# Performance work log

Hardware: AMD Instinct MI355X
Metric: run time of the kernel (lower is better)

The kernel has to match this reference:

```python
import jax, jax.numpy as jnp
from jax import lax
import numpy as np

EPS = 1e-5
K = 16
NUM_GROUP = 128
D = 384
HEADS = 6
DEPTH = 4
BETA = 0.25

def gelu(x):
    return jax.nn.gelu(x, approximate=False)

def linear(x, w, b):
    return x @ w.T + b

def layer_norm(x, g, b):
    mu = x.mean(-1, keepdims=True)
    var = x.var(-1, keepdims=True)
    return (x - mu) / jnp.sqrt(var + EPS) * g + b

def group_norm(x, gamma, beta, groups):
    B, C = x.shape[0], x.shape[1]
    sp = x.shape[2:]
    xg = x.reshape((B, groups, C // groups) + sp)
    axes = tuple(range(2, xg.ndim))
    mu = xg.mean(axes, keepdims=True)
    var = xg.var(axes, keepdims=True)
    xg = (xg - mu) / jnp.sqrt(var + EPS)
    x = xg.reshape((B, C) + sp)
    shp = (1, C) + (1,) * len(sp)
    return x * gamma.reshape(shp) + beta.reshape(shp)

def knn_idx(q, kp, k):
    # q [B,Nq,3], kp [B,Nk,3] -> idx [B,Nq,k] of k nearest keys
    d = jnp.sum(q * q, -1)[:, :, None] - 2.0 * jnp.einsum('bqd,bkd->bqk', q, kp) + jnp.sum(kp * kp, -1)[:, None, :]
    _, idx = lax.top_k(-d, k)
    return idx

def graph_feature(coor_q, x_q, coor_k, x_k, k):
    # coor [B,3,N], x [B,C,N] -> [B,2C,Nq,k]
    idx = knn_idx(coor_q.transpose(0, 2, 1), coor_k.transpose(0, 2, 1), k)
    feat = jax.vmap(lambda a, i: a[:, i])(x_k, idx)  # [B,C,Nq,k]
    xq = x_q[:, :, :, None]
    return jnp.concatenate([feat - xq, jnp.broadcast_to(xq, feat.shape)], axis=1)

def fps_indices(xyz, m):
    # farthest point sampling, start at index 0 (matches pointnet2)
    B, N, _ = xyz.shape
    def body(carry, _):
        dist, far = carry
        c = jnp.take_along_axis(xyz, far[:, None, None], axis=1)
        d = jnp.sum((xyz - c) ** 2, -1)
        dist = jnp.minimum(dist, d)
        return (dist, jnp.argmax(dist, -1).astype(jnp.int32)), far
    init = (jnp.full((B, N), 1e10, xyz.dtype), jnp.zeros((B,), jnp.int32))
    _, idxs = lax.scan(body, init, None, length=m)
    return idxs.T  # [B,m]

def gather_ch(x, idx):
    return jax.vmap(lambda a, i: a[:, i])(x, idx)

def conv1x1_2d(x, w):
    return jnp.einsum('oc,bcnk->bonk', w, x)

def conv1x1_1d(x, w, b):
    return jnp.einsum('oc,bcn->bon', w, x) + b[None, :, None]

def linear_resize(x, out_len):
    # F.interpolate(mode='linear', align_corners=False) along axis 1 of [B,N,D]
    n = x.shape[1]
    pos = (jnp.arange(out_len, dtype=x.dtype) + 0.5) * (n / out_len) - 0.5
    pos = jnp.clip(pos, 0.0, n - 1.0)
    i0 = jnp.floor(pos).astype(jnp.int32)
    i1 = jnp.minimum(i0 + 1, n - 1)
    w = (pos - i0.astype(x.dtype))[None, :, None]
    return x[:, i0] * (1.0 - w) + x[:, i1] * w

def vq(z, cb, beta):
    d = jnp.sum(z * z, -1, keepdims=True) - 2.0 * (z @ cb.T) + jnp.sum(cb * cb, -1)
    eidx = jnp.argmin(d, -1)
    q = cb[eidx]
    loss = jnp.mean((lax.stop_gradient(z) - q) ** 2) + beta * jnp.mean((z - lax.stop_gradient(q)) ** 2)
    q_st = z + lax.stop_gradient(q - z)  # straight-through
    return q_st, loss, eidx

def forward_core(xyz, it_w, it_b, g1_w, g1_g, g1_bt, g2_w, g2_g, g2_bt, g3_w, g3_g, g3_bt, g4_w, g4_g, g4_bt, pe_w1, pe_b1, pe_w2, pe_b2, ip_w1, ip_b1, ip_w2, ip_b2, ln1_g, ln1_b, qkv_w, qkv_b, o_w, o_b, ln2_g, ln2_b, m1_w, m1_b, m2_w, m2_b, pyr_w1, pyr_b1, pyr_g1, pyr_bt1, pyr_w2, pyr_b2, pyr_g2, pyr_bt2, fus_w, fus_b, cb0, cb1, cb2):
    B = xyz.shape[0]
    x = xyz.transpose(0, 2, 1)  # [B,7,N]
    coor, normal, plane = x[:, :3], x[:, 3:6], x[:, 6:7]
    f = conv1x1_1d(coor, it_w, it_b)  # [B,8,N]

    def edge_conv(cq, fq, ck, fk, w, g, bt, groups):
        h = graph_feature(cq, fq, ck, fk, K)
        h = conv1x1_2d(h, w)
        h = group_norm(h, g, bt, groups)
        h = jnp.where(h > 0, h, 0.2 * h)  # LeakyReLU(0.2)
        return h.max(axis=-1)

    f = edge_conv(coor, f, coor, f, g1_w, g1_g, g1_bt, 4)  # [B,32,N]
    idx = fps_indices(coor.transpose(0, 2, 1), NUM_GROUP)
    coor_q, normal_q, plane_q, f_q = gather_ch(coor, idx), gather_ch(normal, idx), gather_ch(plane, idx), gather_ch(f, idx)
    f = edge_conv(coor_q, f_q, coor, f, g2_w, g2_g, g2_bt, 4)  # [B,64,128]
    coor, normal, plane = coor_q, normal_q, plane_q
    f = edge_conv(coor, f, coor, f, g3_w, g3_g, g3_bt, 4)  # [B,64,128]
    idx = fps_indices(coor.transpose(0, 2, 1), NUM_GROUP)
    coor_q, normal_q, plane_q, f_q = gather_ch(coor, idx), gather_ch(normal, idx), gather_ch(plane, idx), gather_ch(f, idx)
    f = edge_conv(coor_q, f_q, coor, f, g4_w, g4_g, g4_bt, 4)  # [B,128,128]
    coor = coor_q.transpose(0, 2, 1)  # [B,128,3]
    f = f.transpose(0, 2, 1)          # [B,128,128]

    pe = linear(gelu(linear(coor, pe_w1, pe_b1)), pe_w2, pe_b2)
    h = linear(gelu(linear(f, ip_w1, ip_b1)), ip_w2, ip_b2)
    t = h + pe
    hd = D // HEADS
    scale = 1.0 / np.sqrt(hd)
    N = t.shape[1]
    for l in range(DEPTH):
        hn = layer_norm(t, ln1_g[l], ln1_b[l])
        qkv = hn @ qkv_w[l] + qkv_b[l]
        q, k_, v = jnp.split(qkv, 3, axis=-1)
        q = q.reshape(B, N, HEADS, hd)
        k_ = k_.reshape(B, N, HEADS, hd)
        v = v.reshape(B, N, HEADS, hd)
        att = jax.nn.softmax(jnp.einsum('bqhd,bkhd->bhqk', q, k_) * scale, axis=-1)
        o = jnp.einsum('bhqk,bkhd->bqhd', att, v).reshape(B, N, D)
        t = t + o @ o_w[l] + o_b[l]
        hn = layer_norm(t, ln2_g[l], ln2_b[l])
        t = t + gelu(hn @ m1_w[l] + m1_b[l]) @ m2_w[l] + m2_b[l]

    base = t  # [B,128,384]
    cbs = (cb0, cb1, cb2)
    outs, losses, idxs = [], [], []
    prev = None
    for level in range(3):
        res = max(base.shape[1] // (2 ** level), 8)
        if res == base.shape[1]:
            lf = base
        else:
            # adaptive_avg_pool1d with evenly dividing bins == reshape-mean
            lf = base.reshape(B, res, base.shape[1] // res, D).mean(2)
        c = lf.transpose(0, 2, 1)
        c = gelu(group_norm(conv1x1_1d(c, pyr_w1[level], pyr_b1[level]), pyr_g1[level], pyr_bt1[level], 8))
        c = gelu(group_norm(conv1x1_1d(c, pyr_w2[level], pyr_b2[level]), pyr_g2[level], pyr_bt2[level], 8))
        proc = c.transpose(0, 2, 1)
        if level > 0:
            pu = prev if prev.shape[1] == res else linear_resize(prev, res)
            proc = gelu(linear(jnp.concatenate([proc, pu], axis=-1), fus_w[level - 1], fus_b[level - 1]))
        q_st, loss, eidx = vq(proc, cbs[level], BETA)
        outs.append(q_st)
        losses.append(loss)
        idxs.append(eidx)
        prev = q_st
    return outs, losses, idxs

def setup_inputs():
    key = jax.random.key(0)
    cnt = [0]
    def nrm(shape, s=0.02):
        cnt[0] += 1
        return jax.random.normal(jax.random.fold_in(key, cnt[0]), shape, jnp.float32) * s
    L = 4
    inp = {}
    inp['xyz'] = nrm((8, 4096, 7), 1.0)
    inp['it_w'] = nrm((8, 3), 0.3)
    inp['it_b'] = jnp.zeros((8,), jnp.float32)
    inp['g1_w'] = nrm((32, 16), 0.1); inp['g1_g'] = jnp.ones((32,)); inp['g1_bt'] = jnp.zeros((32,))
    inp['g2_w'] = nrm((64, 64), 0.1); inp['g2_g'] = jnp.ones((64,)); inp['g2_bt'] = jnp.zeros((64,))
    inp['g3_w'] = nrm((64, 128), 0.1); inp['g3_g'] = jnp.ones((64,)); inp['g3_bt'] = jnp.zeros((64,))
    inp['g4_w'] = nrm((128, 128), 0.1); inp['g4_g'] = jnp.ones((128,)); inp['g4_bt'] = jnp.zeros((128,))
    inp['pe_w1'] = nrm((128, 3), 0.3); inp['pe_b1'] = jnp.zeros((128,))
    inp['pe_w2'] = nrm((D, 128), 0.05); inp['pe_b2'] = jnp.zeros((D,))
    inp['ip_w1'] = nrm((512, 128), 0.05); inp['ip_b1'] = jnp.zeros((512,))
    inp['ip_w2'] = nrm((D, 512), 0.03); inp['ip_b2'] = jnp.zeros((D,))
    inp['ln1_g'] = jnp.ones((L, D)); inp['ln1_b'] = jnp.zeros((L, D))
    inp['qkv_w'] = nrm((L, D, 3 * D)); inp['qkv_b'] = jnp.zeros((L, 3 * D))
    inp['o_w'] = nrm((L, D, D)); inp['o_b'] = jnp.zeros((L, D))
    inp['ln2_g'] = jnp.ones((L, D)); inp['ln2_b'] = jnp.zeros((L, D))
    inp['m1_w'] = nrm((L, D, 4 * D)); inp['m1_b'] = jnp.zeros((L, 4 * D))
    inp['m2_w'] = nrm((L, 4 * D, D)); inp['m2_b'] = jnp.zeros((L, D))
    inp['pyr_w1'] = nrm((3, 2 * D, D), 0.03); inp['pyr_b1'] = jnp.zeros((3, 2 * D))
    inp['pyr_g1'] = jnp.ones((3, 2 * D)); inp['pyr_bt1'] = jnp.zeros((3, 2 * D))
    inp['pyr_w2'] = nrm((3, D, 2 * D), 0.03); inp['pyr_b2'] = jnp.zeros((3, D))
    inp['pyr_g2'] = jnp.ones((3, D)); inp['pyr_bt2'] = jnp.zeros((3, D))
    inp['fus_w'] = nrm((2, D, 2 * D), 0.03); inp['fus_b'] = jnp.zeros((2, D))
    inp['cb0'] = nrm((8192, D), 0.5)
    inp['cb1'] = nrm((4096, D), 0.5)
    inp['cb2'] = nrm((2048, D), 0.5)
    return inp

def reference(xyz, it_w, it_b, g1_w, g1_g, g1_bt, g2_w, g2_g, g2_bt, g3_w, g3_g, g3_bt, g4_w, g4_g, g4_bt, pe_w1, pe_b1, pe_w2, pe_b2, ip_w1, ip_b1, ip_w2, ip_b2, ln1_g, ln1_b, qkv_w, qkv_b, o_w, o_b, ln2_g, ln2_b, m1_w, m1_b, m2_w, m2_b, pyr_w1, pyr_b1, pyr_g1, pyr_bt1, pyr_w2, pyr_b2, pyr_g2, pyr_bt2, fus_w, fus_b, cb0, cb1, cb2):
    outs, losses, idxs = forward_core(xyz, it_w, it_b, g1_w, g1_g, g1_bt, g2_w, g2_g, g2_bt, g3_w, g3_g, g3_bt, g4_w, g4_g, g4_bt, pe_w1, pe_b1, pe_w2, pe_b2, ip_w1, ip_b1, ip_w2, ip_b2, ln1_g, ln1_b, qkv_w, qkv_b, o_w, o_b, ln2_g, ln2_b, m1_w, m1_b, m2_w, m2_b, pyr_w1, pyr_b1, pyr_g1, pyr_bt1, pyr_w2, pyr_b2, pyr_g2, pyr_bt2, fus_w, fus_b, cb0, cb1, cb2)
    # concat quantized features of the 3 levels (128+64+32 tokens), total VQ loss, per-level indices
    return (jnp.concatenate(outs, axis=1), losses[0] + losses[1] + losses[2], idxs[0], idxs[1], idxs[2])
```

## Files before the change

### kernel.cpp

```cpp
#include <hip/hip_runtime.h>
#include <math.h>

#define EPSF 1e-5f

__device__ __forceinline__ float geluf(float x){
  return 0.5f*x*(1.0f + erff(x*0.70710678118654752440f));
}

typedef __attribute__((ext_vector_type(8))) short bf16x8;
typedef __attribute__((ext_vector_type(4))) float f32x4;

constexpr size_t WQKV = 0;
constexpr size_t WO   = WQKV + (size_t)4*1152*384;
constexpr size_t WM1  = WO   + (size_t)4*384*384;
constexpr size_t WM2  = WM1  + (size_t)4*1536*384;
constexpr size_t WIP1 = WM2  + (size_t)4*384*1536;
constexpr size_t WIP2 = WIP1 + (size_t)512*128;
constexpr size_t WPE2 = WIP2 + (size_t)384*512;
constexpr size_t WPY1 = WPE2 + (size_t)384*128;
constexpr size_t WPY2 = WPY1 + (size_t)3*768*384;
constexpr size_t WFUS = WPY2 + (size_t)3*384*768;
constexpr size_t WTOT = WFUS + (size_t)2*384*768;

__device__ __forceinline__ void split_rne(float x, short& h, short& l){
// ... 195 lines not shown
    if(d0 <= tau0){
      int slot = atomicAdd(&scnt[wave][0], 1);
      if(slot < 64){ scd[wave][0][slot] = d0; sci[wave][0][slot] = n; }
    }
    if(d1 <= tau1){
      int slot = atomicAdd(&scnt[wave][1], 1);
      if(slot < 64){ scd[wave][1][slot] = d1; sci[wave][1][slot] = n; }
    }
  }
  __syncthreads();

  #pragma unroll
  for(int qq=0; qq<2; qq++){
    int cnt = scnt[wave][qq];
    int* orow = idxout + ((size_t)b*Nq + nq0 + qq)*KNN_K;
    float nqx = qq ? q1x : q0x;
    float nqy = qq ? q1y : q0y;
    float nqz = qq ? q1z : q0z;
    if(cnt <= 64){
      float d = (lane < cnt) ? scd[wave][qq][lane] : INFINITY;
      int  id = (lane < cnt) ? sci[wave][qq][lane] : 0x7fffffff;
      #pragma unroll
      for(int k=2;k<=64;k<<=1){
        #pragma unroll
        for(int j=k>>1;j>=1;j>>=1){
          float od = __shfl_xor(d, j, 64);
          int oi = __shfl_xor(id, j, 64);
          bool lower = (lane & j)==0;
          bool asc = (lane & k)==0;
          bool otherSmaller = (od < d) || (od==d && oi < id);
          if((lower==asc) == otherSmaller){ d = od; id = oi; }
        }
      }
      if(lane < KNN_K) orow[lane] = id;
    } else {
      float bd[KNN_K]; int bi2[KNN_K];
      #pragma unroll
      for(int j=0;j<KNN_K;j++){ bd[j]=INFINITY; bi2[j]=0x7fffffff; }
      float curmax = INFINITY;
      for(int n=lane; n<Nk; n+=64){
        float4 k4 = sk[n];
        float d = fmaf(nqx, k4.x, fmaf(nqy, k4.y, fmaf(nqz, k4.z, k4.w)));
        if(d < curmax){
          int pm = 0; float md = bd[0]; int mi = bi2[0];
          #pragma unroll
          for(int j=1;j<KNN_K;j++){
            if(bd[j] > md || (bd[j]==md && bi2[j] > mi)){ md=bd[j]; mi=bi2[j]; pm=j; }
          }
          #pragma unroll
          for(int j=0;j<KNN_K;j++){ if(j==pm){ bd[j]=d; bi2[j]=n; } }
          float m2 = -INFINITY;
          #pragma unroll
          for(int j=0;j<KNN_K;j++) m2 = fmaxf(m2, bd[j]);
          curmax = m2;
        }
      }
      for(int t=0;t<KNN_K;t++){
        float ld = bd[0]; int li_ = bi2[0];
        #pragma unroll
        for(int j=1;j<KNN_K;j++){
          if(bd[j] < ld || (bd[j]==ld && bi2[j] < li_)){ ld=bd[j]; li_=bi2[j]; }
        }
        float wd = ld; int wi = li_;
        #pragma unroll
        for(int m=1;m<64;m<<=1){
          float od = __shfl_xor(wd, m, 64);
          int oi = __shfl_xor(wi, m, 64);
          if(od < wd || (od==wd && oi < wi)){ wd=od; wi=oi; }
        }
        if(ld==wd && li_==wi){
          #pragma unroll
          for(int j=0;j<KNN_K;j++){ if(bd[j]==wd && bi2[j]==wi){ bd[j]=INFINITY; bi2[j]=0x7fffffff; } }
        }
        if(lane==0) orow[t] = wi;
      }
    }
  }
}

template<int NMAX, int PPT, int NT>
__global__ __launch_bounds__(NT) void fps_kernel(const float* __restrict__ coor, int* __restrict__ out,
                                                 int N, int M){
  __shared__ float skx[NMAX], sky[NMAX], skz[NMAX];
  __shared__ unsigned long long swk[NT/64];
  constexpr int NW = NT/64;
  int b = blockIdx.x;
  int tid = threadIdx.x;
  int lane = tid & 63, wid = tid >> 6;
  const float* cx = coor + (size_t)b*3*N;
  const float* cy = cx + N;
  const float* cz = cx + 2*N;
  float px[PPT], py[PPT], pz[PPT], dist[PPT];
  #pragma unroll
  for(int j=0;j<PPT;j++){
    int n = tid + j*NT;
    float x = cx[n], y = cy[n], z = cz[n];
    px[j]=x; py[j]=y; pz[j]=z; dist[j]=1e10f;
    skx[n]=x; sky[n]=y; skz[n]=z;
  }
  if(tid==0) out[b*M] = 0;
  __syncthreads();
  float fx = skx[0], fy = sky[0], fz = skz[0];
  for(int t=1;t<M;t++){
    unsigned long long bk = 0ull;
    #pragma unroll
    for(int j=0;j<PPT;j++){
      int n = tid + j*NT;
      float dx = __fsub_rn(px[j], fx);
      float dy = __fsub_rn(py[j], fy);
      float dz = __fsub_rn(pz[j], fz);
      float d = __fadd_rn(__fadd_rn(__fmul_rn(dx,dx), __fmul_rn(dy,dy)), __fmul_rn(dz,dz));
      float nd = fminf(dist[j], d);
      dist[j] = nd;
      union{float f; unsigned u;} db; db.f = nd;
      unsigned long long key = ((unsigned long long)db.u << 32) | (unsigned)(0x7fffffff - n);
      bk = (key > bk) ? key : bk;
    }
    #pragma unroll
    for(int m=1;m<64;m<<=1){
      unsigned long long ok = __shfl_xor(bk, m, 64);
      bk = (ok > bk) ? ok : bk;
    }
    if(lane==0) swk[wid] = bk;
    __syncthreads();
    unsigned long long g = swk[0];
    #pragma unroll
    for(int w=1;w<NW;w++){ unsigned long long o = swk[w]; g = (o > g) ? o : g; }
    int wi = 0x7fffffff - (int)(unsigned)(g & 0xffffffffull);
    if(tid==0) out[b*M + t] = wi;
    fx = skx[wi]; fy = sky[wi]; fz = skz[wi];
    __syncthreads();
  }
}

template<int CIN, int COUT>
__global__ __launch_bounds__(256) void ec_main(const float* __restrict__ fQ, const float* __restrict__ fK,
    const int* __restrict__ idx, const float* __restrict__ W,
    float* __restrict__ hmax_out, float* __restrict__ part, int Nq, int Nk)
{
  constexpr int CG = COUT/4;
  __shared__ float sW1t[CIN][COUT];
  __shared__ float sWdt[CIN][COUT];
  __shared__ float ps[4], pq[4];
  if(threadIdx.x < 4){ ps[threadIdx.x]=0.f; pq[threadIdx.x]=0.f; }
  for(int i=threadIdx.x;i<CIN*COUT;i+=256){
    int c = i % COUT, p = i / COUT;
    float w1 = W[c*2*CIN + p];
    sW1t[p][c] = w1;
    sWdt[p][c] = W[c*2*CIN + CIN + p] - w1;
  }
  __syncthreads();
  int gid = blockIdx.x*256 + threadIdx.x;
  int c = gid % COUT;
  int t = gid / COUT;
  int n = t % Nq;
  int b = t / Nq;
  const float* fq = fQ + ((size_t)b*Nq + n)*CIN;
  float t2 = 0.f;
  #pragma unroll
  for(int p=0;p<CIN;p++) t2 = fmaf(sWdt[p][c], fq[p], t2);
  const int* idr = idx + ((size_t)b*Nq+n)*16;
  const float* fkb = fK + (size_t)b*Nk*CIN;
  float hmax = -INFINITY, s = 0.f, q = 0.f;
  for(int k=0;k<16;k++){
    int nb = idr[k];
    const float* fk = fkb + (size_t)nb*CIN;
    float h = t2;
    #pragma unroll
    for(int p=0;p<CIN;p++) h = fmaf(sW1t[p][c], fk[p], h);
    hmax = fmaxf(hmax, h);
    s += h;
    q = fmaf(h,h,q);
  }
  hmax_out[((size_t)b*Nq + n)*COUT + c] = hmax;
  #pragma unroll
  for(int m=1;m<CG;m<<=1){ s += __shfl_xor(s,m,64); q += __shfl_xor(q,m,64); }
  if((threadIdx.x & (CG-1)) == 0){
    int grp = c / CG;
    atomicAdd(&ps[grp], s);
    atomicAdd(&pq[grp], q);
  }
  __syncthreads();
  if(threadIdx.x < 4){
    part[(size_t)blockIdx.x*8 + threadIdx.x*2+0] = ps[threadIdx.x];
    part[(size_t)blockIdx.x*8 + threadIdx.x*2+1] = pq[threadIdx.x];
  }
}

__global__ __launch_bounds__(256) void ec_reduce(const float* __restrict__ part, float* __restrict__ mr,
                                                 int nblk_per_b, float invcnt){
  int b = blockIdx.x >> 2, g = blockIdx.x & 3;
  const float* p = part + (size_t)b*nblk_per_b*8 + g*2;
  float s=0.f, q=0.f;
  for(int i=threadIdx.x;i<nblk_per_b;i+=256){ s += p[(size_t)i*8]; q += p[(size_t)i*8+1]; }
  __shared__ float rs[256], rq[256];
  rs[threadIdx.x]=s; rq[threadIdx.x]=q; __syncthreads();
  for(int st=128;st>0;st>>=1){
    if(threadIdx.x<st){ rs[threadIdx.x]+=rs[threadIdx.x+st]; rq[threadIdx.x]+=rq[threadIdx.x+st]; }
    __syncthreads();
  }
  if(threadIdx.x==0){
    float mean = rs[0]*invcnt;
    float var = rq[0]*invcnt - mean*mean; var = fmaxf(var, 0.f);
    mr[blockIdx.x*2+0] = mean;
    mr[blockIdx.x*2+1] = 1.0f/sqrtf(var + EPSF);
  }
}

__global__ void ec_norm(float* __restrict__ h, const float* __restrict__ mr, const float* __restrict__ gamma,
                        const float* __restrict__ beta, int Nq, int COUT, int total){
  int i = blockIdx.x*blockDim.x + threadIdx.x;
  if(i >= total) return;
  int c = i % COUT;
  int b = i/(Nq*COUT);
// ... 3 lines not shown
  h[i] = v > 0.f ? v : 0.2f*v;
}

__global__ __launch_bounds__(128) void gemm64(const float* __restrict__ A, const float* __restrict__ Bm,
    const float* __restrict__ bias, float* __restrict__ C,
    int M, int N, int K, int BT, int act, int addto)
{
  __shared__ float As[16][64];
  __shared__ float Bs[16][64];
  int t = threadIdx.x;
  int tx = t & 15, ty = t >> 4;
  int bm = blockIdx.y*64, bn = blockIdx.x*64;
  float acc[8][4] = {{0.f}};
  int kvec = ((K & 15) == 0);
  for(int k0 = 0; k0 < K; k0 += 16){
    #pragma unroll
    for(int i=0;i<2;i++){
      int id = t*2 + i;
      int row = id >> 2, q = id & 3;
      if(kvec){
        float4 av = *(const float4*)(A + (size_t)(bm+row)*K + k0 + q*4);
        As[q*4+0][row]=av.x; As[q*4+1][row]=av.y; As[q*4+2][row]=av.z; As[q*4+3][row]=av.w;
      } else {
        #pragma unroll
        for(int j=0;j<4;j++){
          int kk = k0 + q*4 + j;
          As[q*4+j][row] = (kk < K) ? A[(size_t)(bm+row)*K + kk] : 0.f;
        }
      }
    }
    #pragma unroll
    for(int i=0;i<2;i++){
      int id = t*2 + i;
      if(BT){
        int col = id >> 2, q = id & 3;
        if(kvec){
          float4 bv = *(const float4*)(Bm + (size_t)(bn+col)*K + k0 + q*4);
          Bs[q*4+0][col]=bv.x; Bs[q*4+1][col]=bv.y; Bs[q*4+2][col]=bv.z; Bs[q*4+3][col]=bv.w;
        } else {
          #pragma unroll
          for(int j=0;j<4;j++){
            int kk = k0 + q*4 + j;
            Bs[q*4+j][col] = (kk < K) ? Bm[(size_t)(bn+col)*K + kk] : 0.f;
          }
        }
      } else {
        int kr = id >> 4, cq = (id & 15)*4;
        if(k0+kr < K){
          *(float4*)&Bs[kr][cq] = *(const float4*)(Bm + (size_t)(k0+kr)*N + bn + cq);
        } else {
          Bs[kr][cq]=0.f; Bs[kr][cq+1]=0.f; Bs[kr][cq+2]=0.f; Bs[kr][cq+3]=0.f;
        }
      }
    }
    __syncthreads();
    #pragma unroll
    for(int kk=0;kk<16;kk++){
      float4 a0 = *(const float4*)&As[kk][ty*8];
      float4 a1 = *(const float4*)&As[kk][ty*8+4];
      float4 b  = *(const float4*)&Bs[kk][tx*4];
      float av[8]; float bv[4];
      *(float4*)&av[0] = a0; *(float4*)&av[4] = a1; *(float4*)&bv[0] = b;
      #pragma unroll
      for(int r=0;r<8;r++){
        #pragma unroll
        for(int c2=0;c2<4;c2++) acc[r][c2] = fmaf(av[r], bv[c2], acc[r][c2]);
      }
    }
    __syncthreads();
  }
  float4 bb = make_float4(0.f,0.f,0.f,0.f);
  if(bias) bb = *(const float4*)(bias + bn + tx*4);
  #pragma unroll
  for(int r=0;r<8;r++){
    int row = bm + ty*8 + r;
    float4 v = make_float4(acc[r][0]+bb.x, acc[r][1]+bb.y, acc[r][2]+bb.z, acc[r][3]+bb.w);
    if(act==1){ v.x=geluf(v.x); v.y=geluf(v.y); v.z=geluf(v.z); v.w=geluf(v.w); }
    float* Cp = C + (size_t)row*N + bn + tx*4;
    if(addto){ float4 o = *(const float4*)Cp; v.x+=o.x; v.y+=o.y; v.z+=o.z; v.w+=o.w; }
    *(float4*)Cp = v;
  }
}

__global__ __launch_bounds__(256) void ln_stats(const float* __restrict__ x, float* __restrict__ mr, int D){
  int row = blockIdx.x*4 + (threadIdx.x >> 6);
  int lane = threadIdx.x & 63;
  const float* xr = x + (size_t)row*D;
  float s = 0.f;
  for(int i=lane;i<D;i+=64) s += xr[i];
  #pragma unroll
  for(int m=1;m<64;m<<=1) s += __shfl_xor(s, m, 64);
  float mu = s/(float)D;
  float q = 0.f;
  for(int i=lane;i<D;i+=64){ float d = xr[i]-mu; q += d*d; }
  #pragma unroll
  for(int m=1;m<64;m<<=1) q += __shfl_xor(q, m, 64);
  if(lane==0){
    mr[row*2+0] = mu;
    mr[row*2+1] = 1.0f/sqrtf(q/(float)D + EPSF);
  }
}

__global__ __launch_bounds__(256) void gemm_mfma(const float* __restrict__ A, const float* __restrict__ Bm,
    const float* __restrict__ bias, float* __restrict__ C,
    int M, int N, int K, int BT, int act, int addto,
    const float* __restrict__ lnmr, const float* __restrict__ lng, const float* __restrict__ lnb)
{
  __shared__ short sAhi[64][72];
  __shared__ short sAlo[64][72];
  __shared__ short sBhi[64][72];
  __shared__ short sBlo[64][72];
  int t = threadIdx.x;
  int lane = t & 63, wave = t >> 6;
  int wm = wave >> 1, wn = wave & 1;
  int g = lane >> 4, rr = lane & 15;
  int bm = blockIdx.y*64, bn = blockIdx.x*64;
  f32x4 acc[2][2];
  #pragma unroll
  for(int m=0;m<2;m++)
    #pragma unroll
    for(int n=0;n<2;n++)
      #pragma unroll
      for(int r=0;r<4;r++) acc[m][n][r] = 0.f;

  int ar_ = t >> 2, akq = (t & 3)*16;
  int bc_ = BT ? (t >> 2) : (t & 63);
  int bkq = BT ? ((t & 3)*16) : ((t >> 6)*16);
  float lmu = 0.f, lrstd = 0.f;
  if(lnmr){ lmu = lnmr[(bm+ar_)*2+0]; lrstd = lnmr[(bm+ar_)*2+1]; }

  float areg[16], breg[16];
  auto loadA = [&](int k0){
    const float* ap = A + (size_t)(bm + ar_)*K + k0 + akq;
    *(float4*)&areg[0]  = *(const float4*)(ap);
    *(float4*)&areg[4]  = *(const float4*)(ap+4);
    *(float4*)&areg[8]  = *(const float4*)(ap+8);
    *(float4*)&areg[12] = *(const float4*)(ap+12);
  };
  auto loadB = [&](int k0){
    if(BT){
      const float* bp = Bm + (size_t)(bn + bc_)*K + k0 + bkq;
      *(float4*)&breg[0]  = *(const float4*)(bp);
      *(float4*)&breg[4]  = *(const float4*)(bp+4);
      *(float4*)&breg[8]  = *(const float4*)(bp+8);
      *(float4*)&breg[12] = *(const float4*)(bp+12);
    } else {
      #pragma unroll
      for(int j=0;j<16;j++) breg[j] = Bm[(size_t)(k0 + bkq + j)*N + bn + bc_];
    }
  };
  auto stageA = [&](int k0){
    #pragma unroll
    for(int v8=0; v8<2; v8++){
      bf16x8 h, l;
      #pragma unroll
      for(int j=0;j<8;j++){
        float x = areg[v8*8+j];
        if(lnmr){
          int kk = k0 + akq + v8*8 + j;
          x = (x - lmu)*lrstd*lng[kk] + lnb[kk];
        }
        short th, tl;
        split_rne(x, th, tl);
        h[j] = th; l[j] = tl;
      }
      *(bf16x8*)&sAhi[ar_][akq + v8*8] = h;
      *(bf16x8*)&sAlo[ar_][akq + v8*8] = l;
    }
  };
  auto stageB = [&](){
    #pragma unroll
    for(int v8=0; v8<2; v8++){
      bf16x8 h, l;
      #pragma unroll
      for(int j=0;j<8;j++){
        short th, tl;
        split_rne(breg[v8*8+j], th, tl);
        h[j] = th; l[j] = tl;
      }
      *(bf16x8*)&sBhi[bc_][bkq + v8*8] = h;
      *(bf16x8*)&sBlo[bc_][bkq + v8*8] = l;
    }
  };

  loadA(0); loadB(0);
  int nk = K >> 6;
  for(int ki=0; ki<nk; ki++){
    stageA(ki*64); stageB();
    __syncthreads();
    if(ki+1 < nk){ loadA((ki+1)*64); loadB((ki+1)*64); }
    #pragma unroll
    for(int half=0; half<2; half++){
      bf16x8 ah[2], al[2], bh[2], bl[2];
      #pragma unroll
      for(int m=0;m<2;m++){
        int arow = wm*32 + m*16 + rr;
        ah[m] = *(bf16x8*)&sAhi[arow][half*32 + g*8];
        al[m] = *(bf16x8*)&sAlo[arow][half*32 + g*8];
      }
      #pragma unroll
      for(int n=0;n<2;n++){
        int bcol = wn*32 + n*16 + rr;
        bh[n] = *(bf16x8*)&sBhi[bcol][half*32 + g*8];
        bl[n] = *(bf16x8*)&sBlo[bcol][half*32 + g*8];
      }
      #pragma unroll
      for(int m=0;m<2;m++){
        #pragma unroll
        for(int n=0;n<2;n++){
          acc[m][n] = __builtin_amdgcn_mfma_f32_16x16x32_bf16(ah[m], bh[n], acc[m][n], 0, 0, 0);
          acc[m][n] = __builtin_amdgcn_mfma_f32_16x16x32_bf16(ah[m], bl[n], acc[m][n], 0, 0, 0);
          acc[m][n] = __builtin_amdgcn_mfma_f32_16x16x32_bf16(al[m], bh[n], acc[m][n], 0, 0, 0);
        }
      }
    }
    __syncthreads();
  }
  #pragma unroll
  for(int n=0;n<2;n++){
    int col = bn + wn*32 + n*16 + rr;
    float bb = bias ? bias[col] : 0.f;
    #pragma unroll
    for(int m=0;m<2;m++){
      #pragma unroll
      for(int r4=0;r4<4;r4++){
        int row = bm + wm*32 + m*16 + g*4 + r4;
        float v = acc[m][n][r4] + bb;
        if(act==1) v = geluf(v);
        size_t o = (size_t)row*N + col;
        if(addto) v += C[o];
        C[o] = v;
      }
    }
  }
}

__global__ __launch_bounds__(256) void gemm_mfma_ps(const float* __restrict__ A,
    const short* __restrict__ Bhi, const short* __restrict__ Blo,
    const float* __restrict__ bias, float* __restrict__ C,
    int M, int N, int K, int act, int addto,
    const float* __restrict__ lnmr, const float* __restrict__ lng, const float* __restrict__ lnb)
{
  __shared__ short sAhi[64][72];
  __shared__ short sAlo[64][72];
  __shared__ short sBhi[64][72];
  __shared__ short sBlo[64][72];
  int t = threadIdx.x;
  int lane = t & 63, wave = t >> 6;
  int wm = wave >> 1, wn = wave & 1;
  int g = lane >> 4, rr = lane & 15;
  int bm = blockIdx.y*64, bn = blockIdx.x*64;
  f32x4 acc[2][2];
  #pragma unroll
  for(int m=0;m<2;m++)
    #pragma unroll
    for(int n=0;n<2;n++)
      #pragma unroll
      for(int r=0;r<4;r++) acc[m][n][r] = 0.f;

  int ar_ = t >> 2, akq = (t & 3)*16;
  float lmu = 0.f, lrstd = 0.f;
  if(lnmr){ lmu = lnmr[(bm+ar_)*2+0]; lrstd = lnmr[(bm+ar_)*2+1]; }

  float areg[16];
  bf16x8 pbh[2], pbl[2];
  auto loadA = [&](int k0){
    const float* ap = A + (size_t)(bm + ar_)*K + k0 + akq;
    *(float4*)&areg[0]  = *(const float4*)(ap);
    *(float4*)&areg[4]  = *(const float4*)(ap+4);
    *(float4*)&areg[8]  = *(const float4*)(ap+8);
    *(float4*)&areg[12] = *(const float4*)(ap+12);
  };
  auto loadB = [&](int k0){
    const short* hp = Bhi + (size_t)(bn + ar_)*K + k0 + akq;
    const short* lp = Blo + (size_t)(bn + ar_)*K + k0 + akq;
    pbh[0] = *(const bf16x8*)hp; pbh[1] = *(const bf16x8*)(hp+8);
    pbl[0] = *(const bf16x8*)lp; pbl[1] = *(const bf16x8*)(lp+8);
  };
  auto stageA = [&](int k0){
    #pragma unroll
    for(int v8=0; v8<2; v8++){
      bf16x8 h, l;
      #pragma unroll
      for(int j=0;j<8;j++){
        float x = areg[v8*8+j];
        if(lnmr){
          int kk = k0 + akq + v8*8 + j;
          x = (x - lmu)*lrstd*lng[kk] + lnb[kk];
        }
        short th, tl;
        split_rne(x, th, tl);
        h[j] = th; l[j] = tl;
      }
      *(bf16x8*)&sAhi[ar_][akq + v8*8] = h;
      *(bf16x8*)&sAlo[ar_][akq + v8*8] = l;
    }
  };
  auto stageB = [&](){
    *(bf16x8*)&sBhi[ar_][akq]   = pbh[0];
    *(bf16x8*)&sBhi[ar_][akq+8] = pbh[1];
    *(bf16x8*)&sBlo[ar_][akq]   = pbl[0];
    *(bf16x8*)&sBlo[ar_][akq+8] = pbl[1];
  };

  loadA(0); loadB(0);
  int nk = K >> 6;
  for(int ki=0; ki<nk; ki++){
    stageA(ki*64); stageB();
    __syncthreads();
    if(ki+1 < nk){ loadA((ki+1)*64); loadB((ki+1)*64); }
    #pragma unroll
    for(int half=0; half<2; half++){
      bf16x8 ah[2], al[2], bh[2], bl[2];
      #pragma unroll
      for(int m=0;m<2;m++){
        int arow = wm*32 + m*16 + rr;
        ah[m] = *(bf16x8*)&sAhi[arow][half*32 + g*8];
        al[m] = *(bf16x8*)&sAlo[arow][half*32 + g*8];
      }
      #pragma unroll
      for(int n=0;n<2;n++){
        int bcol = wn*32 + n*16 + rr;
        bh[n] = *(bf16x8*)&sBhi[bcol][half*32 + g*8];
        bl[n] = *(bf16x8*)&sBlo[bcol][half*32 + g*8];
      }
      #pragma unroll
      for(int m=0;m<2;m++){
        #pragma unroll
        for(int n=0;n<2;n++){
          acc[m][n] = __builtin_amdgcn_mfma_f32_16x16x32_bf16(ah[m], bh[n], acc[m][n], 0, 0, 0);
          acc[m][n] = __builtin_amdgcn_mfma_f32_16x16x32_bf16(ah[m], bl[n], acc[m][n], 0, 0, 0);
          acc[m][n] = __builtin_amdgcn_mfma_f32_16x16x32_bf16(al[m], bh[n], acc[m][n], 0, 0, 0);
        }
      }
    }
    __syncthreads();
  }
  #pragma unroll
  for(int n=0;n<2;n++){
    int col = bn + wn*32 + n*16 + rr;
    float bb = bias ? bias[col] : 0.f;
    #pragma unroll
    for(int m=0;m<2;m++){
      #pragma unroll
      for(int r4=0;r4<4;r4++){
        int row = bm + wm*32 + m*16 + g*4 + r4;
        float v = acc[m][n][r4] + bb;
        if(act==1) v = geluf(v);
        size_t o = (size_t)row*N + col;
        if(addto) v += C[o];
        C[o] = v;
      }
    }
  }
}

__global__ __launch_bounds__(256) void gemm_vq(const short* __restrict__ Ahi, const short* __restrict__ Alo,
    const short* __restrict__ Bhi, const short* __restrict__ Blo,
    const float* __restrict__ cbsq, unsigned long long* __restrict__ keys, int M, int N, int K)
{
  __shared__ short sAhi[64][72];
  __shared__ short sAlo[64][72];
  __shared__ short sBhi[64][72];
  __shared__ short sBlo[64][72];
  int t = threadIdx.x;
  int lane = t & 63, wave = t >> 6;
  int wm = wave >> 1, wn = wave & 1;
  int g = lane >> 4, rr = lane & 15;
  int bm = blockIdx.y*64, bn = blockIdx.x*64;
// ... 263 lines not shown
  const float* pyr_w2 = (const float*)d_in[39];
  const float* pyr_b2 = (const float*)d_in[40];
  const float* pyr_g2 = (const float*)d_in[41];
  const float* pyr_bt2= (const float*)d_in[42];
  const float* fus_w  = (const float*)d_in[43];
  const float* fus_b  = (const float*)d_in[44];
  const float* cb0    = (const float*)d_in[45];
  const float* cb1    = (const float*)d_in[46];
  const float* cb2    = (const float*)d_in[47];

  float* ws  = (float*)d_ws;
  float* out = (float*)d_out;

  constexpr int B_ = 8, N0 = 4096, M0 = 128;
  constexpr size_t OFF_COOR0 = 0;
  constexpr size_t OFF_F0    = OFF_COOR0 + (size_t)B_*3*N0;
  constexpr size_t OFF_F1    = OFF_F0 + (size_t)B_*8*N0;
  constexpr size_t OFF_IDX1  = OFF_F1 + (size_t)B_*32*N0;
  constexpr size_t OFF_FPS1  = OFF_IDX1 + (size_t)B_*N0*16;
  constexpr size_t OFF_COOR1 = OFF_FPS1 + B_*M0;
  constexpr size_t OFF_F1Q   = OFF_COOR1 + B_*3*M0;
  constexpr size_t OFF_IDX2  = OFF_F1Q + B_*32*M0;
  constexpr size_t OFF_F2    = OFF_IDX2 + (size_t)B_*M0*16;
  constexpr size_t OFF_IDX3  = OFF_F2 + B_*64*M0;
  constexpr size_t OFF_F3    = OFF_IDX3 + (size_t)B_*M0*16;
  constexpr size_t OFF_FPS2  = OFF_F3 + B_*64*M0;
  constexpr size_t OFF_COOR2 = OFF_FPS2 + B_*M0;
  constexpr size_t OFF_F3Q   = OFF_COOR2 + B_*3*M0;
  constexpr size_t OFF_IDX4  = OFF_F3Q + B_*64*M0;
  constexpr size_t OFF_F4    = OFF_IDX4 + (size_t)B_*M0*16;
  constexpr size_t OFF_COORT = OFF_F4 + B_*128*M0;
  constexpr size_t OFF_TMP   = OFF_COORT + B_*M0*3;
  constexpr size_t OFF_T     = OFF_TMP + (size_t)1024*512;
  constexpr size_t OFF_QKV   = OFF_T + (size_t)1024*384;
  constexpr size_t OFF_ATT   = OFF_QKV + (size_t)1024*1152;
  constexpr size_t OFF_MID   = OFF_ATT + (size_t)1024*384;
  constexpr size_t OFF_LF    = OFF_MID + (size_t)1024*1536;
  constexpr size_t OFF_C1    = OFF_LF + (size_t)512*384;
  constexpr size_t OFF_C2    = OFF_C1 + (size_t)1024*768;
  constexpr size_t OFF_CAT   = OFF_C2 + (size_t)1024*384;
  constexpr size_t OFF_PROC  = OFF_CAT + (size_t)512*768;
  constexpr size_t OFF_KEYS  = OFF_PROC + (size_t)512*384;
  constexpr size_t OFF_LNMR  = OFF_KEYS + 3584;
  constexpr size_t OFF_CBSQ  = OFF_LNMR + 2048;
  constexpr size_t OFF_PART  = OFF_CBSQ + 14336;
  constexpr size_t OFF_MR    = OFF_PART + 32768;
  constexpr size_t OFF_LOSS  = OFF_MR + 64;
  constexpr size_t OFF_ZHI   = OFF_LOSS + 64;
  constexpr size_t OFF_ZLO   = OFF_ZHI + 196608;
  constexpr size_t OFF_CBHI  = OFF_ZLO + 196608;
  constexpr size_t OFF_CBLO  = OFF_CBHI + 2752512;
  constexpr size_t OFF_WHI = OFF_CBLO + 2752512;
  constexpr size_t OFF_WLO = OFF_WHI + (WTOT+1)/2;
  constexpr size_t OFF_END = OFF_WLO + (WTOT+1)/2;

  float* coor0 = ws + OFF_COOR0;
  float* f0    = ws + OFF_F0;
  float* f1    = ws + OFF_F1;
  int*   idx1  = (int*)(ws + OFF_IDX1);
  int*   fps1  = (int*)(ws + OFF_FPS1);
  float* coor1 = ws + OFF_COOR1;
  float* f1q   = ws + OFF_F1Q;
  int*   idx2  = (int*)(ws + OFF_IDX2);
  float* f2    = ws + OFF_F2;
  int*   idx3  = (int*)(ws + OFF_IDX3);
  float* f3    = ws + OFF_F3;
  int*   fps2  = (int*)(ws + OFF_FPS2);
  float* coor2 = ws + OFF_COOR2;
  float* f3q   = ws + OFF_F3Q;
  int*   idx4  = (int*)(ws + OFF_IDX4);
  float* f4    = ws + OFF_F4;
  float* coorT = ws + OFF_COORT;
  float* tmp   = ws + OFF_TMP;
  float* tbuf  = ws + OFF_T;
  float* qkvb  = ws + OFF_QKV;
  float* attb  = ws + OFF_ATT;
  float* midb  = ws + OFF_MID;
  float* lfb   = ws + OFF_LF;
  float* c1b   = ws + OFF_C1;
  float* c2b   = ws + OFF_C2;
  float* catb  = ws + OFF_CAT;
  float* procb = ws + OFF_PROC;
  unsigned long long* keys = (unsigned long long*)(ws + OFF_KEYS);
  float* lnst  = ws + OFF_LNMR;
  float* cbsq  = ws + OFF_CBSQ;
  float* part  = ws + OFF_PART;
  float* mr    = ws + OFF_MR;
  float* lossa = ws + OFF_LOSS;
  short* zhi   = (short*)(ws + OFF_ZHI);
  short* zlo   = (short*)(ws + OFF_ZLO);
  short* cbhi  = (short*)(ws + OFF_CBHI);
  short* cblo  = (short*)(ws + OFF_CBLO);
  short* whi   = (short*)(ws + OFF_WHI);
  short* wlo   = (short*)(ws + OFF_WLO);

  bool presplit = ws_size >= OFF_END * sizeof(float);

  auto cdiv = [](int a, int b){ return (a+b-1)/b; };
  auto gemm_full = [&](const float* A, const float* Bm, const float* bias, float* C,
                       int M, int N, int K, int BT, int act, int addto,
                       const float* lnmr, const float* lng, const float* lnb){
    if(((K & 63) == 0) && ((N & 63) == 0) && ((M & 63) == 0)){
      dim3 g(N/64, M/64);
      gemm_mfma<<<g, 256, 0, stream>>>(A, Bm, bias, C, M, N, K, BT, act, addto, lnmr, lng, lnb);
    } else {
      dim3 g(N/64, M/64), blk(128);
      gemm64<<<g, blk, 0, stream>>>(A, Bm, bias, C, M, N, K, BT, act, addto);
    }
  };
  auto gemmW = [&](const float* A, const float* W, size_t wofs, const float* bias, float* C,
                   int M, int N, int K, int BT, int act, int addto,
                   const float* lnmr, const float* lng, const float* lnb){
    if(presplit && ((K & 63) == 0) && ((N & 63) == 0) && ((M & 63) == 0)){
      dim3 g(N/64, M/64);
      gemm_mfma_ps<<<g, 256, 0, stream>>>(A, whi + wofs, wlo + wofs, bias, C, M, N, K, act, addto, lnmr, lng, lnb);
    } else {
      gemm_full(A, W, bias, C, M, N, K, BT, act, addto, lnmr, lng, lnb);
    }
  };

  hipMemsetAsync(lossa, 0, 8*sizeof(float), stream);
  hipMemsetAsync(keys, 0xFF, 1792*sizeof(unsigned long long), stream);

  init_pts<<<cdiv(B_*N0,256),256,0,stream>>>(xyz, it_w, it_b, coor0, f0, B_, N0);

  split_cb3<<<cdiv(14336*384/4,256),256,0,stream>>>(cb0, cb1, cb2, cbhi, cblo);
  cbsq3<<<cdiv(14336,256),256,0,stream>>>(cb0, cb1, cb2, cbsq);

  if(presplit){
    transpose_split<<<dim3(1152/32,384/32,4),256,0,stream>>>(qkv_w, whi+WQKV, wlo+WQKV, 384, 1152,
        (size_t)384*1152, (size_t)1152*384);
    transpose_split<<<dim3(384/32,384/32,4),256,0,stream>>>(o_w, whi+WO, wlo+WO, 384, 384,
        (size_t)384*384, (size_t)384*384);
    transpose_split<<<dim3(1536/32,384/32,4),256,0,stream>>>(m1_w, whi+WM1, wlo+WM1, 384, 1536,
        (size_t)384*1536, (size_t)1536*384);
    transpose_split<<<dim3(384/32,1536/32,4),256,0,stream>>>(m2_w, whi+WM2, wlo+WM2, 1536, 384,
        (size_t)1536*384, (size_t)384*1536);
    int totq = (512*128 + 384*512 + 384*128 + 3*768*384 + 3*384*768 + 2*384*768)/4;
    split_multi<<<cdiv(totq,256),256,0,stream>>>(ip_w1, ip_w2, pe_w2, pyr_w1, pyr_w2, fus_w, whi, wlo);
  }

  knn2q_kernel<4096,512><<<B_*N0/16,512,0,stream>>>(coor0, coor0, idx1, B_, N0, N0);
  ec_main<8,32><<<B_*32*N0/256,256,0,stream>>>(f0, f0, idx1, g1_w, f1, part, N0, N0);
  ec_reduce<<<32,256,0,stream>>>(part, mr, 32*N0/256, 1.0f/(8.0f*N0*16.0f));
  ec_norm<<<cdiv(B_*32*N0,256),256,0,stream>>>(f1, mr, g1_g, g1_bt, N0, 32, B_*32*N0);

  fps_kernel<4096,8,512><<<B_,512,0,stream>>>(coor0, fps1, N0, M0);
  gather_ch_kernel<<<cdiv(B_*3*M0,256),256,0,stream>>>(coor0, fps1, coor1, B_, 3, N0, M0);
  gather_rows<<<cdiv(B_*M0*32,256),256,0,stream>>>(f1, fps1, f1q, B_, 32, N0, M0);

  knn2q_kernel<4096,512><<<B_*M0/16,512,0,stream>>>(coor1, coor0, idx2, B_, M0, N0);
  ec_main<32,64><<<B_*64*M0/256,256,0,stream>>>(f1q, f1, idx2, g2_w, f2, part, M0, N0);
  ec_reduce<<<32,256,0,stream>>>(part, mr, 64*M0/256, 1.0f/(16.0f*M0*16.0f));
  ec_norm<<<cdiv(B_*64*M0,256),256,0,stream>>>(f2, mr, g2_g, g2_bt, M0, 64, B_*64*M0);

  knn2q_kernel<128,512><<<B_*M0/16,512,0,stream>>>(coor1, coor1, idx3, B_, M0, M0);
  ec_main<64,64><<<B_*64*M0/256,256,0,stream>>>(f2, f2, idx3, g3_w, f3, part, M0, M0);
  ec_reduce<<<32,256,0,stream>>>(part, mr, 64*M0/256, 1.0f/(16.0f*M0*16.0f));
  ec_norm<<<cdiv(B_*64*M0,256),256,0,stream>>>(f3, mr, g3_g, g3_bt, M0, 64, B_*64*M0);

  fps_kernel<128,1,128><<<B_,128,0,stream>>>(coor1, fps2, M0, M0);
  gather_ch_kernel<<<cdiv(B_*3*M0,256),256,0,stream>>>(coor1, fps2, coor2, B_, 3, M0, M0);
  gather_rows<<<cdiv(B_*M0*64,256),256,0,stream>>>(f3, fps2, f3q, B_, 64, M0, M0);

  knn2q_kernel<128,512><<<B_*M0/16,512,0,stream>>>(coor2, coor1, idx4, B_, M0, M0);
  ec_main<64,128><<<B_*128*M0/256,256,0,stream>>>(f3q, f3, idx4, g4_w, f4, part, M0, M0);
  ec_reduce<<<32,256,0,stream>>>(part, mr, 128*M0/256, 1.0f/(32.0f*M0*16.0f));
  ec_norm<<<cdiv(B_*128*M0,256),256,0,stream>>>(f4, mr, g4_g, g4_bt, M0, 128, B_*128*M0);

  transpose_cn<<<cdiv(B_*3*M0,256),256,0,stream>>>(coor2, coorT, B_, 3, M0);

  gemm_full(coorT, pe_w1, pe_b1, tmp, 1024, 128, 3, 1, 1, 0, nullptr, nullptr, nullptr);
  gemmW(tmp, pe_w2, WPE2, pe_b2, tbuf, 1024, 384, 128, 1, 0, 0, nullptr, nullptr, nullptr);
  gemmW(f4, ip_w1, WIP1, ip_b1, tmp, 1024, 512, 128, 1, 1, 0, nullptr, nullptr, nullptr);
  gemmW(tmp, ip_w2, WIP2, ip_b2, tbuf, 1024, 384, 512, 1, 0, 1, nullptr, nullptr, nullptr);

  for(int l=0;l<4;l++){
    ln_stats<<<256,256,0,stream>>>(tbuf, lnst, 384);
    gemmW(tbuf, qkv_w + (size_t)l*384*1152, WQKV + (size_t)l*1152*384, qkv_b + l*1152, qkvb,
          1024, 1152, 384, 0, 0, 0, lnst, ln1_g + l*384, ln1_b + l*384);
    attn_kernel<<<48,128,0,stream>>>(qkvb, attb);
    gemmW(attb, o_w + (size_t)l*384*384, WO + (size_t)l*384*384, o_b + l*384, tbuf,
          1024, 384, 384, 0, 0, 1, nullptr, nullptr, nullptr);
    ln_stats<<<256,256,0,stream>>>(tbuf, lnst, 384);
    gemmW(tbuf, m1_w + (size_t)l*384*1536, WM1 + (size_t)l*1536*384, m1_b + l*1536, midb,
          1024, 1536, 384, 0, 1, 0, lnst, ln2_g + l*384, ln2_b + l*384);
    gemmW(midb, m2_w + (size_t)l*1536*384, WM2 + (size_t)l*384*1536, m2_b + l*384, tbuf,
          1024, 384, 1536, 0, 0, 1, nullptr, nullptr, nullptr);
  }

  const float* cbs[3] = {cb0, cb1, cb2};
  const int ncodes[3] = {8192, 4096, 2048};
  const int cboff[3]  = {0, 8192, 12288};
  const int keyoff[3] = {0, 1024, 1536};
  const int rowoffs[3] = {0, 128, 192};
  const size_t OUT0 = (size_t)8*224*384;
  float* idxouts[3] = { out + OUT0 + 1, out + OUT0 + 1 + 1024, out + OUT0 + 1 + 1536 };

  for(int lv=0; lv<3; ++lv){
    int res = 128 >> lv;
    int rows = 8*res;
    const float* lf;
    if(lv==0){ lf = tbuf; }
    else {
      pool_kernel<<<cdiv(rows*384,256),256,0,stream>>>(tbuf, lfb, B_, res, 1<<lv);
      lf = lfb;
    }
    gemmW(lf, pyr_w1 + (size_t)lv*768*384, WPY1 + (size_t)lv*768*384, pyr_b1 + lv*768, c1b,
          rows, 768, 384, 1, 0, 0, nullptr, nullptr, nullptr);
    gn_gelu_kernel<<<64,256,0,stream>>>(c1b, pyr_g1 + lv*768, pyr_bt1 + lv*768, res, 768, 96);
    gemmW(c1b, pyr_w2 + (size_t)lv*384*768, WPY2 + (size_t)lv*384*768, pyr_b2 + lv*384, c2b,
          rows, 384, 768, 1, 0, 0, nullptr, nullptr, nullptr);
    gn_gelu_kernel<<<64,256,0,stream>>>(c2b, pyr_g2 + lv*384, pyr_bt2 + lv*384, res, 384, 48);
    const float* z = c2b;
    if(lv > 0){
      pu_cat_kernel<<<cdiv(rows*768,256),256,0,stream>>>(c2b, out, catb, B_, res, rowoffs[lv-1]);
      gemmW(catb, fus_w + (size_t)(lv-1)*384*768, WFUS + (size_t)(lv-1)*384*768, fus_b + (lv-1)*384, procb,
            rows, 384, 768, 1, 1, 0, nullptr, nullptr, nullptr);
      z = procb;
    }
    split_planes<<<cdiv(rows*384/4,256),256,0,stream>>>(z, zhi, zlo, rows*384/4);
    gemm_vq<<<dim3(ncodes[lv]/64, rows/64), 256, 0, stream>>>(zhi, zlo,
        cbhi + (size_t)cboff[lv]*384, cblo + (size_t)cboff[lv]*384,
        cbsq + cboff[lv], keys + keyoff[lv], rows, ncodes[lv], 384);
    vq_out_kernel<<<rows,128,0,stream>>>(z, keys + keyoff[lv], cbs[lv], out, lossa + lv, res,
                                         rowoffs[lv], idxouts[lv]);
  }

  loss_kernel<<<1,1,0,stream>>>(lossa, out + OUT0);
}
```

Before: 1.661 ms.

## Fuse layernorm row statistics into GEMM prologue and double-buffer FPS reduction

Removes the separate ln_stats launches (8 per forward) by having each GEMM thread compute the mean and rstd for its A row inside the GEMM, using a 4-lane shuffle reduction over that thread's K-slices. The FPS kernel now writes per-wave maxima into a double-buffered shared array and reduces them with wave shuffles, which lets it drop one __syncthreads per iteration. In exchange, every column block of a LN-fused GEMM rereads its full A rows to recompute the statistics redundantly.

```diff
diff --git a/kernel.cpp b/kernel.cpp
--- a/kernel.cpp
+++ b/kernel.cpp
@@ -301,7 +301,7 @@
 __global__ __launch_bounds__(NT) void fps_kernel(const float* __restrict__ coor, int* __restrict__ out,
                                                  int N, int M){
   __shared__ float skx[NMAX], sky[NMAX], skz[NMAX];
-  __shared__ unsigned long long swk[NT/64];
+  __shared__ unsigned long long swk[2][NT/64];
   constexpr int NW = NT/64;
   int b = blockIdx.x;
   int tid = threadIdx.x;
@@ -340,15 +340,18 @@
       unsigned long long ok = __shfl_xor(bk, m, 64);
       bk = (ok > bk) ? ok : bk;
     }
-    if(lane==0) swk[wid] = bk;
+    int buf = t & 1;
+    if(lane==0) swk[buf][wid] = bk;
     __syncthreads();
-    unsigned long long g = swk[0];
-    #pragma unroll
-    for(int w=1;w<NW;w++){ unsigned long long o = swk[w]; g = (o > g) ? o : g; }
+    unsigned long long g = swk[buf][lane & (NW-1)];
+    #pragma unroll
+    for(int m=1;m<NW;m<<=1){
+      unsigned long long o = __shfl_xor(g, m, 64);
+      g = (o > g) ? o : g;
+    }
     int wi = 0x7fffffff - (int)(unsigned)(g & 0xffffffffull);
     if(tid==0) out[b*M + t] = wi;
     fx = skx[wi]; fy = sky[wi]; fz = skz[wi];
-    __syncthreads();
   }
 }
 
@@ -518,29 +521,45 @@
   }
 }
 
-__global__ __launch_bounds__(256) void ln_stats(const float* __restrict__ x, float* __restrict__ mr, int D){
-  int row = blockIdx.x*4 + (threadIdx.x >> 6);
-  int lane = threadIdx.x & 63;
-  const float* xr = x + (size_t)row*D;
+__device__ __forceinline__ void ln_row_stats(const float* __restrict__ A, int row, int K, int akq,
+                                             float& lmu, float& lrstd){
+  const float* ap = A + (size_t)row*K + akq;
   float s = 0.f;
-  for(int i=lane;i<D;i+=64) s += xr[i];
-  #pragma unroll
-  for(int m=1;m<64;m<<=1) s += __shfl_xor(s, m, 64);
-  float mu = s/(float)D;
+  for(int k0 = 0; k0 < K; k0 += 64){
+    float4 v0 = *(const float4*)(ap + k0);
+    float4 v1 = *(const float4*)(ap + k0 + 4);
+    float4 v2 = *(const float4*)(ap + k0 + 8);
+    float4 v3 = *(const float4*)(ap + k0 + 12);
+    s += v0.x+v0.y+v0.z+v0.w + v1.x+v1.y+v1.z+v1.w + v2.x+v2.y+v2.z+v2.w + v3.x+v3.y+v3.z+v3.w;
+  }
+  s += __shfl_xor(s, 1, 64);
+  s += __shfl_xor(s, 2, 64);
+  lmu = s / (float)K;
   float q = 0.f;
-  for(int i=lane;i<D;i+=64){ float d = xr[i]-mu; q += d*d; }
-  #pragma unroll
-  for(int m=1;m<64;m<<=1) q += __shfl_xor(q, m, 64);
-  if(lane==0){
-    mr[row*2+0] = mu;
-    mr[row*2+1] = 1.0f/sqrtf(q/(float)D + EPSF);
-  }
+  for(int k0 = 0; k0 < K; k0 += 64){
+    float4 v0 = *(const float4*)(ap + k0);
+    float4 v1 = *(const float4*)(ap + k0 + 4);
+    float4 v2 = *(const float4*)(ap + k0 + 8);
+    float4 v3 = *(const float4*)(ap + k0 + 12);
+    float t0;
+    t0 = v0.x-lmu; q = fmaf(t0,t0,q); t0 = v0.y-lmu; q = fmaf(t0,t0,q);
+    t0 = v0.z-lmu; q = fmaf(t0,t0,q); t0 = v0.w-lmu; q = fmaf(t0,t0,q);
+    t0 = v1.x-lmu; q = fmaf(t0,t0,q); t0 = v1.y-lmu; q = fmaf(t0,t0,q);
+    t0 = v1.z-lmu; q = fmaf(t0,t0,q); t0 = v1.w-lmu; q = fmaf(t0,t0,q);
+    t0 = v2.x-lmu; q = fmaf(t0,t0,q); t0 = v2.y-lmu; q = fmaf(t0,t0,q);
+    t0 = v2.z-lmu; q = fmaf(t0,t0,q); t0 = v2.w-lmu; q = fmaf(t0,t0,q);
+    t0 = v3.x-lmu; q = fmaf(t0,t0,q); t0 = v3.y-lmu; q = fmaf(t0,t0,q);
+    t0 = v3.z-lmu; q = fmaf(t0,t0,q); t0 = v3.w-lmu; q = fmaf(t0,t0,q);
+  }
+  q += __shfl_xor(q, 1, 64);
+  q += __shfl_xor(q, 2, 64);
+  lrstd = 1.0f/sqrtf(q/(float)K + EPSF);
 }
 
 __global__ __launch_bounds__(256) void gemm_mfma(const float* __restrict__ A, const float* __restrict__ Bm,
     const float* __restrict__ bias, float* __restrict__ C,
     int M, int N, int K, int BT, int act, int addto,
-    const float* __restrict__ lnmr, const float* __restrict__ lng, const float* __restrict__ lnb)
+    const float* __restrict__ lng, const float* __restrict__ lnb)
 {
   __shared__ short sAhi[64][72];
   __shared__ short sAlo[64][72];
@@ -563,7 +582,7 @@
   int bc_ = BT ? (t >> 2) : (t & 63);
   int bkq = BT ? ((t & 3)*16) : ((t >> 6)*16);
   float lmu = 0.f, lrstd = 0.f;
-  if(lnmr){ lmu = lnmr[(bm+ar_)*2+0]; lrstd = lnmr[(bm+ar_)*2+1]; }
+  if(lng) ln_row_stats(A, bm + ar_, K, akq, lmu, lrstd);
 
   float areg[16], breg[16];
   auto loadA = [&](int k0){
@@ -592,7 +611,7 @@
       #pragma unroll
       for(int j=0;j<8;j++){
         float x = areg[v8*8+j];
-        if(lnmr){
+        if(lng){
           int kk = k0 + akq + v8*8 + j;
           x = (x - lmu)*lrstd*lng[kk] + lnb[kk];
         }
@@ -675,7 +694,7 @@
     const short* __restrict__ Bhi, const short* __restrict__ Blo,
     const float* __restrict__ bias, float* __restrict__ C,
     int M, int N, int K, int act, int addto,
-    const float* __restrict__ lnmr, const float* __restrict__ lng, const float* __restrict__ lnb)
+    const float* __restrict__ lng, const float* __restrict__ lnb)
 {
   __shared__ short sAhi[64][72];
   __shared__ short sAlo[64][72];
@@ -696,7 +715,7 @@
 
   int ar_ = t >> 2, akq = (t & 3)*16;
   float lmu = 0.f, lrstd = 0.f;
-  if(lnmr){ lmu = lnmr[(bm+ar_)*2+0]; lrstd = lnmr[(bm+ar_)*2+1]; }
+  if(lng) ln_row_stats(A, bm + ar_, K, akq, lmu, lrstd);
 
   float areg[16];
   bf16x8 pbh[2], pbl[2];
@@ -720,7 +739,7 @@
       #pragma unroll
       for(int j=0;j<8;j++){
         float x = areg[v8*8+j];
-        if(lnmr){
+        if(lng){
           int kk = k0 + akq + v8*8 + j;
           x = (x - lmu)*lrstd*lng[kk] + lnb[kk];
         }
@@ -1150,7 +1169,6 @@
   float* catb  = ws + OFF_CAT;
   float* procb = ws + OFF_PROC;
   unsigned long long* keys = (unsigned long long*)(ws + OFF_KEYS);
-  float* lnst  = ws + OFF_LNMR;
   float* cbsq  = ws + OFF_CBSQ;
   float* part  = ws + OFF_PART;
   float* mr    = ws + OFF_MR;
@@ -1167,10 +1185,10 @@
   auto cdiv = [](int a, int b){ return (a+b-1)/b; };
   auto gemm_full = [&](const float* A, const float* Bm, const float* bias, float* C,
                        int M, int N, int K, int BT, int act, int addto,
-                       const float* lnmr, const float* lng, const float* lnb){
+                       const float* lng, const float* lnb){
     if(((K & 63) == 0) && ((N & 63) == 0) && ((M & 63) == 0)){
       dim3 g(N/64, M/64);
-      gemm_mfma<<<g, 256, 0, stream>>>(A, Bm, bias, C, M, N, K, BT, act, addto, lnmr, lng, lnb);
+      gemm_mfma<<<g, 256, 0, stream>>>(A, Bm, bias, C, M, N, K, BT, act, addto, lng, lnb);
     } else {
       dim3 g(N/64, M/64), blk(128);
       gemm64<<<g, blk, 0, stream>>>(A, Bm, bias, C, M, N, K, BT, act, addto);
@@ -1178,12 +1196,12 @@
   };
   auto gemmW = [&](const float* A, const float* W, size_t wofs, const float* bias, float* C,
                    int M, int N, int K, int BT, int act, int addto,
-                   const float* lnmr, const float* lng, const float* lnb){
+                   const float* lng, const float* lnb){
     if(presplit && ((K & 63) == 0) && ((N & 63) == 0) && ((M & 63) == 0)){
       dim3 g(N/64, M/64);
-      gemm_mfma_ps<<<g, 256, 0, stream>>>(A, whi + wofs, wlo + wofs, bias, C, M, N, K, act, addto, lnmr, lng, lnb);
+      gemm_mfma_ps<<<g, 256, 0, stream>>>(A, whi + wofs, wlo + wofs, bias, C, M, N, K, act, addto, lng, lnb);
     } else {
-      gemm_full(A, W, bias, C, M, N, K, BT, act, addto, lnmr, lng, lnb);
+      gemm_full(A, W, bias, C, M, N, K, BT, act, addto, lng, lnb);
     }
   };
 
@@ -1238,23 +1256,21 @@
 
   transpose_cn<<<cdiv(B_*3*M0,256),256,0,stream>>>(coor2, coorT, B_, 3, M0);
 
-  gemm_full(coorT, pe_w1, pe_b1, tmp, 1024, 128, 3, 1, 1, 0, nullptr, nullptr, nullptr);
-  gemmW(tmp, pe_w2, WPE2, pe_b2, tbuf, 1024, 384, 128, 1, 0, 0, nullptr, nullptr, nullptr);
-  gemmW(f4, ip_w1, WIP1, ip_b1, tmp, 1024, 512, 128, 1, 1, 0, nullptr, nullptr, nullptr);
-  gemmW(tmp, ip_w2, WIP2, ip_b2, tbuf, 1024, 384, 512, 1, 0, 1, nullptr, nullptr, nullptr);
+  gemm_full(coorT, pe_w1, pe_b1, tmp, 1024, 128, 3, 1, 1, 0, nullptr, nullptr);
+  gemmW(tmp, pe_w2, WPE2, pe_b2, tbuf, 1024, 384, 128, 1, 0, 0, nullptr, nullptr);
+  gemmW(f4, ip_w1, WIP1, ip_b1, tmp, 1024, 512, 128, 1, 1, 0, nullptr, nullptr);
+  gemmW(tmp, ip_w2, WIP2, ip_b2, tbuf, 1024, 384, 512, 1, 0, 1, nullptr, nullptr);
 
   for(int l=0;l<4;l++){
-    ln_stats<<<256,256,0,stream>>>(tbuf, lnst, 384);
     gemmW(tbuf, qkv_w + (size_t)l*384*1152, WQKV + (size_t)l*1152*384, qkv_b + l*1152, qkvb,
-          1024, 1152, 384, 0, 0, 0, lnst, ln1_g + l*384, ln1_b + l*384);
+          1024, 1152, 384, 0, 0, 0, ln1_g + l*384, ln1_b + l*384);
     attn_kernel<<<48,128,0,stream>>>(qkvb, attb);
     gemmW(attb, o_w + (size_t)l*384*384, WO + (size_t)l*384*384, o_b + l*384, tbuf,
-          1024, 384, 384, 0, 0, 1, nullptr, nullptr, nullptr);
-    ln_stats<<<256,256,0,stream>>>(tbuf, lnst, 384);
+          1024, 384, 384, 0, 0, 1, nullptr, nullptr);
     gemmW(tbuf, m1_w + (size_t)l*384*1536, WM1 + (size_t)l*1536*384, m1_b + l*1536, midb,
-          1024, 1536, 384, 0, 1, 0, lnst, ln2_g + l*384, ln2_b + l*384);
+          1024, 1536, 384, 0, 1, 0, ln2_g + l*384, ln2_b + l*384);
     gemmW(midb, m2_w + (size_t)l*1536*384, WM2 + (size_t)l*384*1536, m2_b + l*384, tbuf,
-          1024, 384, 1536, 0, 0, 1, nullptr, nullptr, nullptr);
+          1024, 384, 1536, 0, 0, 1, nullptr, nullptr);
   }
 
   const float* cbs[3] = {cb0, cb1, cb2};
@@ -1275,16 +1291,16 @@
       lf = lfb;
     }
     gemmW(lf, pyr_w1 + (size_t)lv*768*384, WPY1 + (size_t)lv*768*384, pyr_b1 + lv*768, c1b,
-          rows, 768, 384, 1, 0, 0, nullptr, nullptr, nullptr);
+          rows, 768, 384, 1, 0, 0, nullptr, nullptr);
     gn_gelu_kernel<<<64,256,0,stream>>>(c1b, pyr_g1 + lv*768, pyr_bt1 + lv*768, res, 768, 96);
     gemmW(c1b, pyr_w2 + (size_t)lv*384*768, WPY2 + (size_t)lv*384*768, pyr_b2 + lv*384, c2b,
-          rows, 384, 768, 1, 0, 0, nullptr, nullptr, nullptr);
+          rows, 384, 768, 1, 0, 0, nullptr, nullptr);
     gn_gelu_kernel<<<64,256,0,stream>>>(c2b, pyr_g2 + lv*384, pyr_bt2 + lv*384, res, 384, 48);
     const float* z = c2b;
     if(lv > 0){
       pu_cat_kernel<<<cdiv(rows*768,256),256,0,stream>>>(c2b, out, catb, B_, res, rowoffs[lv-1]);
       gemmW(catb, fus_w + (size_t)(lv-1)*384*768, WFUS + (size_t)(lv-1)*384*768, fus_b + (lv-1)*384, procb,
-            rows, 384, 768, 1, 1, 0, nullptr, nullptr, nullptr);
+            rows, 384, 768, 1, 1, 0, nullptr, nullptr);
       z = procb;
     }
     split_planes<<<cdiv(rows*384/4,256),256,0,stream>>>(z, zhi, zlo, rows*384/4);
```

Measured after the change: 1.621 ms. 1.02x faster.
